# Kernel tuning notes

Measured on AMD Instinct MI355X. Metric: run time of the kernel, lower is better.

The kernel has to match this reference:

```python
import jax, jax.numpy as jnp
import numpy as np

QMAX = 7.0  # 4-bit symmetric: levels in [-8, 7]

def quant4(w):
    # per-tensor symmetric 4-bit fake-quant with straight-through estimator
    s = jnp.max(jnp.abs(w)) / QMAX
    q = jnp.clip(jnp.round(w / s), -8.0, 7.0) * s
    return w + jax.lax.stop_gradient(q - w)

def setup_inputs() -> dict:
    key = jax.random.key(0)
    ks = jax.random.split(key, 7)
    B = 2048
    x = jax.random.normal(ks[0], (B, 1, 31, 16, 31), dtype=jnp.float32)
    # conv: out_ch=1, in_ch=1, kernel (5,3,5)
    w_conv = jax.random.normal(ks[1], (1, 1, 5, 3, 5), dtype=jnp.float32) * 0.1
    b_conv = jax.random.normal(ks[2], (1,), dtype=jnp.float32) * 0.1
    w_fc1 = jax.random.normal(ks[3], (128, 343), dtype=jnp.float32) * 0.05
    b_fc1 = jax.random.normal(ks[4], (128,), dtype=jnp.float32) * 0.05
    w_fc2 = jax.random.normal(ks[5], (4, 128), dtype=jnp.float32) * 0.05
    b_fc2 = jax.random.normal(ks[6], (4,), dtype=jnp.float32) * 0.05
    return {"x": x, "w_conv": w_conv, "b_conv": b_conv,
            "w_fc1": w_fc1, "b_fc1": b_fc1, "w_fc2": w_fc2, "b_fc2": b_fc2}

def reference(x, w_conv, b_conv, w_fc1, b_fc1, w_fc2, b_fc2):
    # QuantConv3d: 4-bit quantized weights, stride (2,1,2), no padding
    c1 = jax.lax.conv_general_dilated(
        x, quant4(w_conv), window_strides=(2, 1, 2), padding='VALID',
        dimension_numbers=('NCDHW', 'OIDHW', 'NCDHW'))
    c1 = c1 + b_conv.reshape(1, -1, 1, 1, 1)          # [B,1,14,14,14]
    # MaxPool3d(2)
    p1 = jax.lax.reduce_window(c1, -jnp.inf, jax.lax.max,
                               (1, 1, 2, 2, 2), (1, 1, 2, 2, 2), 'VALID')  # [B,1,7,7,7]
    f = p1.reshape(p1.shape[0], -1)                   # [B,343]
    a1 = jax.nn.relu(f @ quant4(w_fc1).T + b_fc1)     # [B,128]
    s2 = a1 @ quant4(w_fc2).T + b_fc2                 # [B,4]
    return jax.nn.softmax(s2, axis=1)
```

## Files before the change

### kernel.cpp

```cpp
#include <hip/hip_runtime.h>

#define WS_WCONV   128
#define WS_W1T     256
#define WS_W2      44160

__device__ __forceinline__ float q4(float w, float s) {
  if (s <= 0.f) return 0.f;
  float r = rintf(w / s);
  r = fminf(fmaxf(r, -8.f), 7.f);
  return r * s;
}

__global__ __launch_bounds__(256) void quant_all(
    const float* __restrict__ wconv, const float* __restrict__ w1,
    const float* __restrict__ w2, float* __restrict__ ws) {
  __shared__ float red[256];
  int b = blockIdx.x, t = threadIdx.x;
  if (b < 88) {
    const float4* w4 = (const float4*)w1;
    float m = 0.f;
    for (int i = t; i < 10976; i += 256) {
      float4 v = w4[i];
      m = fmaxf(m, fmaxf(fmaxf(fabsf(v.x), fabsf(v.y)),
                         fmaxf(fabsf(v.z), fabsf(v.w))));
    }
    red[t] = m;
    __syncthreads();
    for (int s = 128; s > 0; s >>= 1) {
      if (t < s) red[t] = fmaxf(red[t], red[t + s]);
      __syncthreads();
    }
    float s = red[0] * (1.0f / 7.0f);
    #pragma unroll
    for (int k = 0; k < 2; ++k) {
      int idx = b * 512 + k * 256 + t;
      if (idx < 43904) {
        float q = q4(w1[idx], s);
        int o = idx / 343;
        int j = idx - o * 343;
        ws[WS_W1T + j * 128 + o] = q;
      }
    }
  } else {
    float mc = (t < 75) ? fabsf(wconv[t]) : 0.f;
    float m2 = 0.f;
    for (int i = t; i < 512; i += 256) m2 = fmaxf(m2, fabsf(w2[i]));
    red[t] = mc;
    __syncthreads();
    for (int s = 128; s > 0; s >>= 1) {
      if (t < s) red[t] = fmaxf(red[t], red[t + s]);
      __syncthreads();
    }
    float sc = red[0] * (1.0f / 7.0f);
    __syncthreads();
    red[t] = m2;
    __syncthreads();
    for (int s = 128; s > 0; s >>= 1) {
      if (t < s) red[t] = fmaxf(red[t], red[t + s]);
      __syncthreads();
    }
    float s2 = red[0] * (1.0f / 7.0f);
    if (t < 75) ws[WS_WCONV + t] = q4(wconv[t], sc);
    #pragma unroll
    for (int k = 0; k < 2; ++k) {
      int idx = k * 256 + t;
      ws[WS_W2 + idx] = q4(w2[idx], s2);
    }
  }
}

__device__ __forceinline__ void conv_all(
    const float* __restrict__ xs, const float* __restrict__ wq,
    int t, float bc, float* __restrict__ feat) {
  if (t >= 343) return;
  int pdl = t / 49;
  int rr  = t - pdl * 49;
  int ph  = rr / 7;
  int pw  = rr - ph * 7;
  float c[2][2][2];
  #pragma unroll
  for (int i = 0; i < 8; ++i) ((float*)c)[i] = 0.f;
  int base0 = pdl * 1984 + ph * 62 + pw * 4;
  #pragma unroll
  for (int dd = 0; dd < 7; ++dd) {
    int rbase = base0 + dd * 496;
    #pragma unroll
    for (int hh = 0; hh < 4; ++hh) {
      float row[7];
      #pragma unroll
      for (int wi = 0; wi < 7; ++wi) row[wi] = xs[rbase + hh * 31 + wi];
      #pragma unroll
      for (int odp = 0; odp < 2; ++odp) {
        int kd = dd - 2 * odp;
        if (kd < 0 || kd > 4) continue;
        #pragma unroll
        for (int ohp = 0; ohp < 2; ++ohp) {
          int kh = hh - ohp;
          if (kh < 0 || kh > 2) continue;
          #pragma unroll
          for (int owp = 0; owp < 2; ++owp) {
            float a = c[odp][ohp][owp];
            #pragma unroll
            for (int kw = 0; kw < 5; ++kw)
              a = fmaf(row[2 * owp + kw], wq[kd * 15 + kh * 5 + kw], a);
            c[odp][ohp][owp] = a;
          }
        }
      }
    }
  }
  float m = ((float*)c)[0];
  #pragma unroll
  for (int i = 1; i < 8; ++i) m = fmaxf(m, ((float*)c)[i]);
  feat[pdl * 49 + rr] = m + bc;
}

__global__ __launch_bounds__(384) void fused_net(
    const float* __restrict__ x, const float* __restrict__ bconv,
    const float* __restrict__ ws, const float* __restrict__ bfc1,
    const float* __restrict__ bfc2, float* __restrict__ out) {
  __shared__ alignas(16) float xs[15376];
  __shared__ alignas(16) float feat[344];
  float* fc1p = xs;
  float* a1   = xs + 128;
  float* s2   = xs + 256;
  int t = threadIdx.x;
  int b = blockIdx.x;
  const float* wq = ws + WS_WCONV;
  float bc = bconv[0];

  {
    const float4* src = (const float4*)(x + (size_t)b * 15376);
    float4* dst = (float4*)xs;
    for (int i = t; i < 3844; i += 384) dst[i] = src[i];
    if (t == 0) feat[343] = 0.f;
  }
  __syncthreads();

  conv_all(xs, wq, t, bc, feat);
  __syncthreads();

  int g = (t >> 7) & 1, o = t & 127;
  float acc = 0.f;
  if (t < 256) {
    const float* w1T = ws + WS_W1T;
    int j0 = g ? 172 : 0;
    const float4* f4 = (const float4*)&feat[j0];
    const float* wp = w1T + j0 * 128 + o;
    float q0 = 0.f, q1 = 0.f, q2 = 0.f, q3 = 0.f;
    for (int q = 0; q < 43; ++q) {
      float4 ff = f4[q];
      q0 = fmaf(ff.x, wp[0],   q0);
      q1 = fmaf(ff.y, wp[128], q1);
      q2 = fmaf(ff.z, wp[256], q2);
      q3 = fmaf(ff.w, wp[384], q3);
      wp += 512;
    }
    acc = (q0 + q1) + (q2 + q3);
    if (g) fc1p[o] = acc;
  }
  __syncthreads();
  if (t < 256 && !g) a1[o] = fmaxf(acc + fc1p[o] + bfc1[o], 0.f);
  __syncthreads();

  if (t < 64) {
    int cls = t & 3, kk = t >> 2;
    const float* w2p = ws + WS_W2 + cls * 128 + kk * 8;
    const float* av = a1 + kk * 8;
    float p = 0.f;
    #pragma unroll
    for (int i = 0; i < 8; ++i) p = fmaf(av[i], w2p[i], p);
    p += __shfl_down(p, 32);
    p += __shfl_down(p, 16);
    p += __shfl_down(p, 8);
    p += __shfl_down(p, 4);
    if (t < 4) s2[t] = p + bfc2[t];
  }
  __syncthreads();
  if (t < 4) {
    float v0 = s2[0], v1 = s2[1], v2 = s2[2], v3 = s2[3];
    float m = fmaxf(fmaxf(v0, v1), fmaxf(v2, v3));
    float e0 = expf(v0 - m), e1 = expf(v1 - m);
    float e2 = expf(v2 - m), e3 = expf(v3 - m);
    float inv = 1.f / (e0 + e1 + e2 + e3);
    float mine = (t == 0) ? e0 : (t == 1) ? e1 : (t == 2) ? e2 : e3;
    out[b * 4 + t] = mine * inv;
  }
}

extern "C" void kernel_launch(void* const* d_in, const int* in_sizes, int n_in,
                              void* d_out, int out_size, void* d_ws, size_t ws_size,
                              hipStream_t stream) {
  const float* x     = (const float*)d_in[0];
  const float* wconv = (const float*)d_in[1];
  const float* bconv = (const float*)d_in[2];
  const float* wfc1  = (const float*)d_in[3];
  const float* bfc1  = (const float*)d_in[4];
  const float* wfc2  = (const float*)d_in[5];
  const float* bfc2  = (const float*)d_in[6];
  float* out = (float*)d_out;
  float* ws  = (float*)d_ws;

  quant_all<<<89, 256, 0, stream>>>(wconv, wfc1, wfc2, ws);
  fused_net<<<2048, 384, 0, stream>>>(x, bconv, ws, bfc1, bfc2, out);
}
```

Measured before the change: 263.1 us.

## Process input volume in depth chunks to shrink shared memory and raise occupancy

```diff
diff --git a/kernel.cpp b/kernel.cpp
--- a/kernel.cpp
+++ b/kernel.cpp
@@ -69,10 +69,10 @@
   }
 }
 
-__device__ __forceinline__ void conv_all(
+__device__ __forceinline__ void conv_phase(
     const float* __restrict__ xs, const float* __restrict__ wq,
-    int t, float bc, float* __restrict__ feat) {
-  if (t >= 343) return;
+    int t, int npf, int pd_off, float bc, float* __restrict__ feat) {
+  if (t >= npf) return;
   int pdl = t / 49;
   int rr  = t - pdl * 49;
   int ph  = rr / 7;
@@ -112,14 +112,14 @@
   float m = ((float*)c)[0];
   #pragma unroll
   for (int i = 1; i < 8; ++i) m = fmaxf(m, ((float*)c)[i]);
-  feat[pdl * 49 + rr] = m + bc;
-}
-
-__global__ __launch_bounds__(384) void fused_net(
+  feat[(pdl + pd_off) * 49 + rr] = m + bc;
+}
+
+__global__ __launch_bounds__(256, 4) void fused_net(
     const float* __restrict__ x, const float* __restrict__ bconv,
     const float* __restrict__ ws, const float* __restrict__ bfc1,
     const float* __restrict__ bfc2, float* __restrict__ out) {
-  __shared__ alignas(16) float xs[15376];
+  __shared__ alignas(16) float xs[5456];
   __shared__ alignas(16) float feat[344];
   float* fc1p = xs;
   float* a1   = xs + 128;
@@ -128,21 +128,32 @@
   int b = blockIdx.x;
   const float* wq = ws + WS_WCONV;
   float bc = bconv[0];
-
+  const float4* xb4 = (const float4*)(x + (size_t)b * 15376);
+  float4* dst = (float4*)xs;
+
+  for (int i = t; i < 1364; i += 256) dst[i] = xb4[i];
+  if (t == 0) feat[343] = 0.f;
+  __syncthreads();
+  conv_phase(xs, wq, t, 98, 0, bc, feat);
+  __syncthreads();
+
+  for (int i = t; i < 1364; i += 256) dst[i] = xb4[992 + i];
+  __syncthreads();
+  conv_phase(xs, wq, t, 98, 2, bc, feat);
+  __syncthreads();
+
+  for (int i = t; i < 1364; i += 256) dst[i] = xb4[1984 + i];
+  __syncthreads();
+  conv_phase(xs, wq, t, 98, 4, bc, feat);
+  __syncthreads();
+
+  for (int i = t; i < 868; i += 256) dst[i] = xb4[2976 + i];
+  __syncthreads();
+  conv_phase(xs, wq, t, 49, 6, bc, feat);
+  __syncthreads();
+
+  int g = t >> 7, o = t & 127;
   {
-    const float4* src = (const float4*)(x + (size_t)b * 15376);
-    float4* dst = (float4*)xs;
-    for (int i = t; i < 3844; i += 384) dst[i] = src[i];
-    if (t == 0) feat[343] = 0.f;
-  }
-  __syncthreads();
-
-  conv_all(xs, wq, t, bc, feat);
-  __syncthreads();
-
-  int g = (t >> 7) & 1, o = t & 127;
-  float acc = 0.f;
-  if (t < 256) {
     const float* w1T = ws + WS_W1T;
     int j0 = g ? 172 : 0;
     const float4* f4 = (const float4*)&feat[j0];
@@ -156,11 +167,11 @@
       q3 = fmaf(ff.w, wp[384], q3);
       wp += 512;
     }
-    acc = (q0 + q1) + (q2 + q3);
+    float acc = (q0 + q1) + (q2 + q3);
     if (g) fc1p[o] = acc;
-  }
-  __syncthreads();
-  if (t < 256 && !g) a1[o] = fmaxf(acc + fc1p[o] + bfc1[o], 0.f);
+    __syncthreads();
+    if (!g) a1[o] = fmaxf(acc + fc1p[o] + bfc1[o], 0.f);
+  }
   __syncthreads();
 
   if (t < 64) {
@@ -202,5 +213,5 @@
   float* ws  = (float*)d_ws;
 
   quant_all<<<89, 256, 0, stream>>>(wconv, wfc1, wfc2, ws);
-  fused_net<<<2048, 384, 0, stream>>>(x, bconv, ws, bfc1, bfc2, out);
-}
+  fused_net<<<2048, 256, 0, stream>>>(x, bconv, ws, bfc1, bfc2, out);
+}
```

Result: faster. 234.9 us (-10.7%).

## Read conv input directly from global memory instead of staging in LDS

Applied to the files above, without the earlier changes.

```diff
diff --git a/kernel.cpp b/kernel.cpp
--- a/kernel.cpp
+++ b/kernel.cpp
@@ -69,8 +69,10 @@
   }
 }
 
-__device__ __forceinline__ void conv_all(
-    const float* __restrict__ xs, const float* __restrict__ wq,
+struct __align__(4) f4u { float x, y, z, w; };
+
+__device__ __forceinline__ void conv_global(
+    const float* __restrict__ xb, const float* __restrict__ wq,
     int t, float bc, float* __restrict__ feat) {
   if (t >= 343) return;
   int pdl = t / 49;
@@ -80,15 +82,16 @@
   float c[2][2][2];
   #pragma unroll
   for (int i = 0; i < 8; ++i) ((float*)c)[i] = 0.f;
-  int base0 = pdl * 1984 + ph * 62 + pw * 4;
+  const float* b0 = xb + pdl * 1984 + ph * 62 + pw * 4;
   #pragma unroll
   for (int dd = 0; dd < 7; ++dd) {
-    int rbase = base0 + dd * 496;
+    const float* rb = b0 + dd * 496;
     #pragma unroll
     for (int hh = 0; hh < 4; ++hh) {
-      float row[7];
-      #pragma unroll
-      for (int wi = 0; wi < 7; ++wi) row[wi] = xs[rbase + hh * 31 + wi];
+      const float* rp = rb + hh * 31;
+      f4u A = *(const f4u*)rp;
+      f4u B = *(const f4u*)(rp + 3);
+      float row[7] = {A.x, A.y, A.z, A.w, B.y, B.z, B.w};
       #pragma unroll
       for (int odp = 0; odp < 2; ++odp) {
         int kd = dd - 2 * odp;
@@ -115,29 +118,22 @@
   feat[pdl * 49 + rr] = m + bc;
 }
 
-__global__ __launch_bounds__(384) void fused_net(
+__global__ __launch_bounds__(384, 6) void fused_net(
     const float* __restrict__ x, const float* __restrict__ bconv,
     const float* __restrict__ ws, const float* __restrict__ bfc1,
     const float* __restrict__ bfc2, float* __restrict__ out) {
-  __shared__ alignas(16) float xs[15376];
   __shared__ alignas(16) float feat[344];
-  float* fc1p = xs;
-  float* a1   = xs + 128;
-  float* s2   = xs + 256;
+  __shared__ alignas(16) float fc1p[128];
+  __shared__ alignas(16) float a1[128];
+  __shared__ float s2[4];
   int t = threadIdx.x;
   int b = blockIdx.x;
   const float* wq = ws + WS_WCONV;
   float bc = bconv[0];
-
-  {
-    const float4* src = (const float4*)(x + (size_t)b * 15376);
-    float4* dst = (float4*)xs;
-    for (int i = t; i < 3844; i += 384) dst[i] = src[i];
-    if (t == 0) feat[343] = 0.f;
-  }
-  __syncthreads();
-
-  conv_all(xs, wq, t, bc, feat);
+  const float* xb = x + (size_t)b * 15376;
+
+  if (t == 383) feat[343] = 0.f;
+  conv_global(xb, wq, t, bc, feat);
   __syncthreads();
 
   int g = (t >> 7) & 1, o = t & 127;
```

Result: faster. 243.4 us (-7.5%).
